# Performance work log

Measured on AMD Instinct MI355X. Metric: run time of the kernel, lower is better.

The kernel has to match this reference:

```python
import math
import jax, jax.numpy as jnp
import numpy as np

HEAD_DIM = 2
ROPE_PERIOD = 19.0
OMEGA = 2.0 * math.pi / ROPE_PERIOD
PEAK_EPS = 0.3
TARGET_LOGIT_GAP = math.log(10.0)
ATTN_AMPLITUDE = TARGET_LOGIT_GAP / (math.cos(OMEGA * PEAK_EPS) - math.cos(OMEGA * (1.0 - PEAK_EPS)))
QK_NORM_SCALE = math.sqrt(ATTN_AMPLITUDE / math.sqrt(2.0))
SCALE = HEAD_DIM ** (-0.5) * QK_NORM_SCALE ** 2
INTERMEDIATE_SIZE = 2
EMBED_CONST = 1000.0
B, L = 4, 4096


def _rms(x, eps=1e-6):
    return x * jax.lax.rsqrt(jnp.mean(x * x, axis=-1, keepdims=True) + eps)


def _rope(x):
    # x: (B, 1, L, 2)
    seq_len = x.shape[2]
    theta = jnp.arange(seq_len, dtype=x.dtype) * jnp.asarray(OMEGA, x.dtype)
    cos_t = jnp.cos(theta)[None, None, :, None]
    sin_t = jnp.sin(theta)[None, None, :, None]
    x0, x1 = x[..., 0:1], x[..., 1:2]
    return jnp.concatenate([x0 * cos_t - x1 * sin_t, x0 * sin_t + x1 * cos_t], axis=-1)


def setup_inputs() -> dict:
    key = jax.random.key(0)
    k1, k2, k3, k4, k5 = jax.random.split(key, 5)
    x = jax.random.normal(k1, (B, L, 2), dtype=jnp.float32)
    # causal additive mask (1, 1, L, L)
    causal = jnp.tril(jnp.ones((L, L), dtype=bool))
    mask = jnp.where(causal, 0.0, -1e9).astype(jnp.float32)[None, None]
    q_weight = jax.random.normal(k2, (1,), dtype=jnp.float32) * 0.1
    v_weight = jax.random.normal(k3, (1,), dtype=jnp.float32) * 0.1
    gate_weight = jax.random.normal(k4, (2,), dtype=jnp.float32) * 0.1
    carry_weight = jax.random.normal(k5, (1,), dtype=jnp.float32) * 0.1
    return {"x": x, "mask": mask, "q_weight": q_weight, "v_weight": v_weight,
            "gate_weight": gate_weight, "carry_weight": carry_weight}


def reference(x, mask, q_weight, v_weight, gate_weight, carry_weight):
    # ---- attention branch ----
    xn = _rms(x)                                    # (B, L, 2)
    phi = q_weight[0]
    q = jnp.stack([xn[..., 0] * jnp.cos(phi), xn[..., 0] * -jnp.sin(phi)], axis=-1)
    k = jnp.stack([xn[..., 0], jnp.zeros_like(xn[..., 0])], axis=-1)
    v = jnp.stack([xn[..., 1] * v_weight[0], jnp.zeros_like(xn[..., 0])], axis=-1)
    q, k, v = q[:, None], k[:, None], v[:, None]    # (B, 1, L, 2)
    q = _rope(_rms(q))
    k = _rope(_rms(k))
    attn = jnp.einsum('bhqd,bhkd->bhqk', q, k) * jnp.asarray(SCALE, x.dtype)
    attn = jax.nn.softmax(attn + mask, axis=-1)
    out = jnp.einsum('bhqk,bhkd->bhqd', attn, v)    # (B, 1, L, 2)
    o0 = out[:, 0, :, 0]                            # (B, L)
    attn_out = jnp.stack([jnp.zeros_like(o0), o0], axis=-1)  # OProj channel swap
    h = x + attn_out
    # ---- gated MLP branch ----
    hn = _rms(h)
    a, c = gate_weight[0], gate_weight[1]
    g0 = hn[..., 0] * a + hn[..., 1] * c
    g1 = hn[..., 0] * (a - c / EMBED_CONST) + hn[..., 1] * c
    base = hn[..., 0]
    mix0 = jax.nn.silu(g0) * base
    mix1 = jax.nn.silu(g1) * base
    y1 = carry_weight[0] * (mix1 - mix0)
    mlp_out = jnp.stack([jnp.zeros_like(y1), y1], axis=-1)
    return h + mlp_out
```

## Files before the change

### kernel.cpp

```cpp
#include <hip/hip_runtime.h>
#include <hip/hip_fp16.h>
#include <math.h>

#define SEQ_L 4096
#define THREADS 512
#define WAVES 8
#define BLOCKS_PER_BATCH 256

__global__ __launch_bounds__(THREADS, 8) void attn_rows_kernel(
    const float* __restrict__ x,
    const float* __restrict__ q_weight,
    const float* __restrict__ v_weight,
    const float* __restrict__ gate_weight,
    const float* __restrict__ carry_weight,
    float* __restrict__ out,
    float scaleL2,
    float cd, float sd,
    float ck1, float sk1,
    float ck2, float sk2,
    float ck3, float sk3)
{
    __shared__ __half2 aw[SEQ_L];

    const int tid  = threadIdx.x;
    const int lane = tid & 63;
    const int wave = tid >> 6;
    const int b    = blockIdx.x >> 8;
    const int bb   = blockIdx.x & 255;

    const float phi = q_weight[0];
    const float vw  = v_weight[0];
    const float2* x2 = (const float2*)x + (size_t)b * SEQ_L;

    const float INV2PI = 0.15915494309189535f;
    const float rphi = phi * INV2PI;
    const float cphi = __builtin_amdgcn_cosf(rphi);
    const float sphi = __builtin_amdgcn_sinf(rphi);

    for (int j = tid; j < SEQ_L; j += THREADS) {
        float2 xv = x2[j];
        float inv = __builtin_amdgcn_rsqf(
                        fmaf(xv.x, xv.x * 0.5f, fmaf(xv.y, xv.y * 0.5f, 1e-6f)));
        float xn0 = xv.x * inv;
        float xn1 = xv.y * inv;
        float a = xn0 * __builtin_amdgcn_rsqf(fmaf(xn0, xn0 * 0.5f, 1e-6f));
        aw[j] = __floats2half2_rn(a, xn1 * vw);
    }
    __syncthreads();

    const float ga = gate_weight[0];
    const float gc = gate_weight[1];
    const float cw = carry_weight[0];

    const int v = bb * WAVES + wave;
    const float SQRT2 = 1.4142135623730951f;
    const float LOG2E = 1.4426950408889634f;
    const float INV19 = 1.0f / 19.0f;

    #pragma unroll
    for (int rr = 0; rr < 2; ++rr) {
        const int i = (rr == 0) ? v : (SEQ_L - 1 - v);

        const float2 xv = x2[i];
        float invx = __builtin_amdgcn_rsqf(
                        fmaf(xv.x, xv.x * 0.5f, fmaf(xv.y, xv.y * 0.5f, 1e-6f)));
        float xn0i = xv.x * invx;
        float a_i  = xn0i * __builtin_amdgcn_rsqf(fmaf(xn0i, xn0i * 0.5f, 1e-6f));
        const float t2 = scaleL2 * a_i;
        const float M2 = fabsf(t2) * SQRT2;

        unsigned r = (unsigned)(i - (lane << 2) + 266) % 19u;
        float rev = (float)r * INV19;
        float cr = __builtin_amdgcn_cosf(rev);
        float sr = __builtin_amdgcn_sinf(rev);
        float c0 = fmaf(sr, sphi, cr * cphi);
        float s0 = fmaf(cr, -sphi, sr * cphi);
        float C = t2 * c0;
        float S = t2 * s0;

        float sA = 0.f, sB = 0.f, oA = 0.f, oB = 0.f;
        int jb = lane << 2;
        const int nfull = (i + 1) >> 8;

        for (int k = 0; k < nfull; ++k) {
            float4 raw = *(const float4*)&aw[jb];
            const __half2* hp = (const __half2*)&raw;
            float2 p0 = __half22float2(hp[0]);
            float2 p1 = __half22float2(hp[1]);
            float2 p2 = __half22float2(hp[2]);
            float2 p3 = __half22float2(hp[3]);
            float C1 = fmaf(S, sk1, C * ck1);
            float C2 = fmaf(S, sk2, C * ck2);
            float C3 = fmaf(S, sk3, C * ck3);
            float e0 = __builtin_amdgcn_exp2f(fmaf(p0.x, C,  -M2));
            float e1 = __builtin_amdgcn_exp2f(fmaf(p1.x, C1, -M2));
            float e2 = __builtin_amdgcn_exp2f(fmaf(p2.x, C2, -M2));
            float e3 = __builtin_amdgcn_exp2f(fmaf(p3.x, C3, -M2));
            sA += e0 + e1;
            sB += e2 + e3;
            oA = fmaf(e0, p0.y, oA);
            oB = fmaf(e1, p1.y, oB);
            oA = fmaf(e2, p2.y, oA);
            oB = fmaf(e3, p3.y, oB);
            float Cn = fmaf(S, sd, C * cd);
            float Sn = fmaf(S, cd, -(C * sd));
            C = Cn; S = Sn;
            jb += 256;
        }
        if ((i & 255) != 255) {
            float4 raw = *(const float4*)&aw[jb];
            const __half2* hp = (const __half2*)&raw;
            float2 p0 = __half22float2(hp[0]);
            float2 p1 = __half22float2(hp[1]);
            float2 p2 = __half22float2(hp[2]);
            float2 p3 = __half22float2(hp[3]);
            float C1 = fmaf(S, sk1, C * ck1);
            float C2 = fmaf(S, sk2, C * ck2);
            float C3 = fmaf(S, sk3, C * ck3);
            float e0 = __builtin_amdgcn_exp2f(fmaf(p0.x, C,  -M2));
            float e1 = __builtin_amdgcn_exp2f(fmaf(p1.x, C1, -M2));
            float e2 = __builtin_amdgcn_exp2f(fmaf(p2.x, C2, -M2));
            float e3 = __builtin_amdgcn_exp2f(fmaf(p3.x, C3, -M2));
            e0 = (jb + 0 <= i) ? e0 : 0.f;
            e1 = (jb + 1 <= i) ? e1 : 0.f;
            e2 = (jb + 2 <= i) ? e2 : 0.f;
            e3 = (jb + 3 <= i) ? e3 : 0.f;
            sA += e0 + e1;
            sB += e2 + e3;
            oA = fmaf(e0, p0.y, oA);
            oB = fmaf(e1, p1.y, oB);
            oA = fmaf(e2, p2.y, oA);
            oB = fmaf(e3, p3.y, oB);
        }

        float ssum = sA + sB;
        float osum = oA + oB;
        for (int off = 32; off > 0; off >>= 1) {
            ssum += __shfl_xor(ssum, off);
            osum += __shfl_xor(osum, off);
        }

        if (lane == 0) {
            float o0 = osum * __builtin_amdgcn_rcpf(ssum);
            float h0 = xv.x;
            float h1 = xv.y + o0;
            float inv = __builtin_amdgcn_rsqf(
                           fmaf(h0, h0 * 0.5f, fmaf(h1, h1 * 0.5f, 1e-6f)));
            float hn0 = h0 * inv, hn1 = h1 * inv;
            float g0 = hn0 * ga + hn1 * gc;
            float g1 = hn0 * (ga - gc * 1e-3f) + hn1 * gc;
            float sig0 = __builtin_amdgcn_rcpf(1.f + __builtin_amdgcn_exp2f(-g0 * LOG2E));
            float sig1 = __builtin_amdgcn_rcpf(1.f + __builtin_amdgcn_exp2f(-g1 * LOG2E));
            float mix0 = g0 * sig0 * hn0;
            float mix1 = g1 * sig1 * hn0;
            float y1 = cw * (mix1 - mix0);
            float2* outp = (float2*)out + (size_t)b * SEQ_L + i;
            *outp = make_float2(xv.x, h1 + y1);
        }
    }
}

extern "C" void kernel_launch(void* const* d_in, const int* in_sizes, int n_in,
                              void* d_out, int out_size, void* d_ws, size_t ws_size,
                              hipStream_t stream)
{
    const float* x  = (const float*)d_in[0];
    const float* qw = (const float*)d_in[2];
    const float* vw = (const float*)d_in[3];
    const float* gw = (const float*)d_in[4];
    const float* cw = (const float*)d_in[5];
    float* out = (float*)d_out;

    const double omega = 2.0 * M_PI / 19.0;
    const double amp   = log(10.0) / (cos(omega * 0.3) - cos(omega * 0.7));
    const double qkns2 = amp / sqrt(2.0);
    const double scale = pow(2.0, -0.5) * qkns2;
    const double L2E   = 1.4426950408889634074;
    const double delta = 256.0 * omega;

    attn_rows_kernel<<<dim3(4 * BLOCKS_PER_BATCH), dim3(THREADS), 0, stream>>>(
        x, qw, vw, gw, cw, out,
        (float)(scale * L2E),
        (float)cos(delta),       (float)sin(delta),
        (float)cos(omega),       (float)sin(omega),
        (float)cos(2.0 * omega), (float)sin(2.0 * omega),
        (float)cos(3.0 * omega), (float)sin(3.0 * omega));
}
```

Before: 19.22 us.

## Process four rows sharing RoPE phase per wave to reuse key loads and rotations

Each wave now handles a group of four query rows whose indices differ by multiples of 19, so they share the same RoPE phase. One set of key loads and cosine rotations then serves all four rows, and the per-row scale folds into a single fma. Groups are paired from both ends of the sequence to balance causal work, the grid is halved with launch bounds relaxed to 4, and the wave reductions use DPP instead of shuffles. In exchange each thread carries more accumulators, which raises register pressure, and the odd group count needs special handling by two waves.

```diff
diff --git a/kernel.cpp b/kernel.cpp
--- a/kernel.cpp
+++ b/kernel.cpp
@@ -4,10 +4,149 @@
 
 #define SEQ_L 4096
 #define THREADS 512
-#define WAVES 8
-#define BLOCKS_PER_BATCH 256
-
-__global__ __launch_bounds__(THREADS, 8) void attn_rows_kernel(
+
+__device__ __forceinline__ float wave_sum_dpp(float x) {
+    int t;
+    t = __builtin_amdgcn_update_dpp(0, __float_as_int(x), 0x111, 0xf, 0xf, true); x += __int_as_float(t);
+    t = __builtin_amdgcn_update_dpp(0, __float_as_int(x), 0x112, 0xf, 0xf, true); x += __int_as_float(t);
+    t = __builtin_amdgcn_update_dpp(0, __float_as_int(x), 0x114, 0xf, 0xf, true); x += __int_as_float(t);
+    t = __builtin_amdgcn_update_dpp(0, __float_as_int(x), 0x118, 0xf, 0xf, true); x += __int_as_float(t);
+    t = __builtin_amdgcn_update_dpp(0, __float_as_int(x), 0x142, 0xa, 0xf, true); x += __int_as_float(t);
+    t = __builtin_amdgcn_update_dpp(0, __float_as_int(x), 0x143, 0xc, 0xf, true); x += __int_as_float(t);
+    return x;
+}
+
+__device__ __forceinline__ void do_group(
+    int g, int lane, const float2* __restrict__ x2, const __half2* aw,
+    float2* __restrict__ outp, float scaleL2, float cphi, float sphi,
+    float cd, float sd, float ck1, float sk1, float ck2, float sk2,
+    float ck3, float sk3, float ga, float gc, float cw)
+{
+    const float INV19 = 1.0f / 19.0f;
+    const float LOG2E = 1.4426950408889634f;
+
+    int m  = g / 19;
+    int c  = g - 19 * m;
+    int b0 = 76 * m + c;
+    int i0r = b0, i1r = b0 + 19, i2r = b0 + 38, i3r = b0 + 57;
+
+    float t2a0, t2a1, t2a2, t2a3, M2a0, M2a1, M2a2, M2a3;
+#define ROWINIT(tk, Mk, ik) { \
+    int ic_ = (ik) < SEQ_L ? (ik) : (SEQ_L - 1); \
+    float2 xv_ = x2[ic_]; \
+    float inv_ = __builtin_amdgcn_rsqf(fmaf(xv_.x, xv_.x*0.5f, fmaf(xv_.y, xv_.y*0.5f, 1e-6f))); \
+    float xn0_ = xv_.x * inv_; \
+    float ai_  = xn0_ * __builtin_amdgcn_rsqf(fmaf(xn0_, xn0_*0.5f, 1e-6f)); \
+    tk = scaleL2 * ai_;  Mk = fabsf(tk) * 1.4142135623730951f; }
+    ROWINIT(t2a0, M2a0, i0r)
+    ROWINIT(t2a1, M2a1, i1r)
+    ROWINIT(t2a2, M2a2, i2r)
+    ROWINIT(t2a3, M2a3, i3r)
+#undef ROWINIT
+
+    unsigned r = (unsigned)(b0 - (lane << 2) + 266) % 19u;
+    float rev = (float)r * INV19;
+    float crv = __builtin_amdgcn_cosf(rev);
+    float srv = __builtin_amdgcn_sinf(rev);
+    float C = fmaf(srv, sphi, crv * cphi);
+    float S = fmaf(crv, -sphi, srv * cphi);
+
+    float sa0=0.f, sa1=0.f, sa2=0.f, sa3=0.f;
+    float oa0=0.f, oa1=0.f, oa2=0.f, oa3=0.f;
+    int jb = lane << 2;
+    const int ncom = (b0 + 1) >> 8;
+    const int i3c  = i3r < SEQ_L ? i3r : (SEQ_L - 1);
+    const int T    = (i3c >> 8) + 1;
+
+#define EL(u, pw) { \
+    float e0_ = __builtin_amdgcn_exp2f(fmaf(t2a0, (u), -M2a0)); \
+    float e1_ = __builtin_amdgcn_exp2f(fmaf(t2a1, (u), -M2a1)); \
+    float e2_ = __builtin_amdgcn_exp2f(fmaf(t2a2, (u), -M2a2)); \
+    float e3_ = __builtin_amdgcn_exp2f(fmaf(t2a3, (u), -M2a3)); \
+    sa0 += e0_; oa0 = fmaf(e0_, (pw), oa0); \
+    sa1 += e1_; oa1 = fmaf(e1_, (pw), oa1); \
+    sa2 += e2_; oa2 = fmaf(e2_, (pw), oa2); \
+    sa3 += e3_; oa3 = fmaf(e3_, (pw), oa3); }
+#define ELM(u, pw, jj) { \
+    float e0_ = __builtin_amdgcn_exp2f(fmaf(t2a0, (u), -M2a0)); \
+    float e1_ = __builtin_amdgcn_exp2f(fmaf(t2a1, (u), -M2a1)); \
+    float e2_ = __builtin_amdgcn_exp2f(fmaf(t2a2, (u), -M2a2)); \
+    float e3_ = __builtin_amdgcn_exp2f(fmaf(t2a3, (u), -M2a3)); \
+    e0_ = ((jj) <= i0r) ? e0_ : 0.f; \
+    e1_ = ((jj) <= i1r) ? e1_ : 0.f; \
+    e2_ = ((jj) <= i2r) ? e2_ : 0.f; \
+    e3_ = ((jj) <= i3r) ? e3_ : 0.f; \
+    sa0 += e0_; oa0 = fmaf(e0_, (pw), oa0); \
+    sa1 += e1_; oa1 = fmaf(e1_, (pw), oa1); \
+    sa2 += e2_; oa2 = fmaf(e2_, (pw), oa2); \
+    sa3 += e3_; oa3 = fmaf(e3_, (pw), oa3); }
+
+    int t = 0;
+    for (; t < ncom; ++t) {
+        float4 raw = *(const float4*)&aw[jb];
+        const __half2* hp = (const __half2*)&raw;
+        float2 p0 = __half22float2(hp[0]);
+        float2 p1 = __half22float2(hp[1]);
+        float2 p2 = __half22float2(hp[2]);
+        float2 p3 = __half22float2(hp[3]);
+        float C1 = fmaf(S, sk1, C * ck1);
+        float C2 = fmaf(S, sk2, C * ck2);
+        float C3 = fmaf(S, sk3, C * ck3);
+        float u0 = p0.x * C,  u1 = p1.x * C1, u2 = p2.x * C2, u3 = p3.x * C3;
+        EL(u0, p0.y) EL(u1, p1.y) EL(u2, p2.y) EL(u3, p3.y)
+        float Cn = fmaf(S, sd, C * cd);
+        float Sn = fmaf(S, cd, -(C * sd));
+        C = Cn; S = Sn;
+        jb += 256;
+    }
+    for (; t < T; ++t) {
+        float4 raw = *(const float4*)&aw[jb];
+        const __half2* hp = (const __half2*)&raw;
+        float2 p0 = __half22float2(hp[0]);
+        float2 p1 = __half22float2(hp[1]);
+        float2 p2 = __half22float2(hp[2]);
+        float2 p3 = __half22float2(hp[3]);
+        float C1 = fmaf(S, sk1, C * ck1);
+        float C2 = fmaf(S, sk2, C * ck2);
+        float C3 = fmaf(S, sk3, C * ck3);
+        float u0 = p0.x * C,  u1 = p1.x * C1, u2 = p2.x * C2, u3 = p3.x * C3;
+        ELM(u0, p0.y, jb)     ELM(u1, p1.y, jb + 1)
+        ELM(u2, p2.y, jb + 2) ELM(u3, p3.y, jb + 3)
+        float Cn = fmaf(S, sd, C * cd);
+        float Sn = fmaf(S, cd, -(C * sd));
+        C = Cn; S = Sn;
+        jb += 256;
+    }
+#undef EL
+#undef ELM
+
+    float S0 = wave_sum_dpp(sa0), O0 = wave_sum_dpp(oa0);
+    float S1 = wave_sum_dpp(sa1), O1 = wave_sum_dpp(oa1);
+    float S2 = wave_sum_dpp(sa2), O2 = wave_sum_dpp(oa2);
+    float S3 = wave_sum_dpp(sa3), O3 = wave_sum_dpp(oa3);
+
+    if (lane == 63) {
+#define EPI(Sk, Ok, ik) if ((ik) < SEQ_L) { \
+    float2 xv_ = x2[ik]; \
+    float o0_ = (Ok) * __builtin_amdgcn_rcpf(Sk); \
+    float h0_ = xv_.x, h1_ = xv_.y + o0_; \
+    float inv_ = __builtin_amdgcn_rsqf(fmaf(h0_, h0_*0.5f, fmaf(h1_, h1_*0.5f, 1e-6f))); \
+    float hn0_ = h0_ * inv_, hn1_ = h1_ * inv_; \
+    float g0_ = hn0_ * ga + hn1_ * gc; \
+    float g1_ = hn0_ * (ga - gc * 1e-3f) + hn1_ * gc; \
+    float sg0_ = __builtin_amdgcn_rcpf(1.f + __builtin_amdgcn_exp2f(-g0_ * LOG2E)); \
+    float sg1_ = __builtin_amdgcn_rcpf(1.f + __builtin_amdgcn_exp2f(-g1_ * LOG2E)); \
+    float y1_ = cw * (g1_ * sg1_ - g0_ * sg0_) * hn0_; \
+    outp[ik] = make_float2(h0_, h1_ + y1_); }
+        EPI(S0, O0, i0r)
+        EPI(S1, O1, i1r)
+        EPI(S2, O2, i2r)
+        EPI(S3, O3, i3r)
+#undef EPI
+    }
+}
+
+__global__ __launch_bounds__(THREADS, 4) void attn_rows_kernel(
     const float* __restrict__ x,
     const float* __restrict__ q_weight,
     const float* __restrict__ v_weight,
@@ -16,21 +155,20 @@
     float* __restrict__ out,
     float scaleL2,
     float cd, float sd,
-    float ck1, float sk1,
-    float ck2, float sk2,
-    float ck3, float sk3)
+    float ck1, float sk1, float ck2, float sk2, float ck3, float sk3)
 {
     __shared__ __half2 aw[SEQ_L];
 
     const int tid  = threadIdx.x;
     const int lane = tid & 63;
     const int wave = tid >> 6;
-    const int b    = blockIdx.x >> 8;
-    const int bb   = blockIdx.x & 255;
+    const int bat  = blockIdx.x >> 7;
+    const int bb   = blockIdx.x & 127;
 
     const float phi = q_weight[0];
     const float vw  = v_weight[0];
-    const float2* x2 = (const float2*)x + (size_t)b * SEQ_L;
+    const float2* x2 = (const float2*)x + (size_t)bat * SEQ_L;
+    float2* outp = (float2*)out + (size_t)bat * SEQ_L;
 
     const float INV2PI = 0.15915494309189535f;
     const float rphi = phi * INV2PI;
@@ -52,112 +190,17 @@
     const float gc = gate_weight[1];
     const float cw = carry_weight[0];
 
-    const int v = bb * WAVES + wave;
-    const float SQRT2 = 1.4142135623730951f;
-    const float LOG2E = 1.4426950408889634f;
-    const float INV19 = 1.0f / 19.0f;
-
-    #pragma unroll
-    for (int rr = 0; rr < 2; ++rr) {
-        const int i = (rr == 0) ? v : (SEQ_L - 1 - v);
-
-        const float2 xv = x2[i];
-        float invx = __builtin_amdgcn_rsqf(
-                        fmaf(xv.x, xv.x * 0.5f, fmaf(xv.y, xv.y * 0.5f, 1e-6f)));
-        float xn0i = xv.x * invx;
-        float a_i  = xn0i * __builtin_amdgcn_rsqf(fmaf(xn0i, xn0i * 0.5f, 1e-6f));
-        const float t2 = scaleL2 * a_i;
-        const float M2 = fabsf(t2) * SQRT2;
-
-        unsigned r = (unsigned)(i - (lane << 2) + 266) % 19u;
-        float rev = (float)r * INV19;
-        float cr = __builtin_amdgcn_cosf(rev);
-        float sr = __builtin_amdgcn_sinf(rev);
-        float c0 = fmaf(sr, sphi, cr * cphi);
-        float s0 = fmaf(cr, -sphi, sr * cphi);
-        float C = t2 * c0;
-        float S = t2 * s0;
-
-        float sA = 0.f, sB = 0.f, oA = 0.f, oB = 0.f;
-        int jb = lane << 2;
-        const int nfull = (i + 1) >> 8;
-
-        for (int k = 0; k < nfull; ++k) {
-            float4 raw = *(const float4*)&aw[jb];
-            const __half2* hp = (const __half2*)&raw;
-            float2 p0 = __half22float2(hp[0]);
-            float2 p1 = __half22float2(hp[1]);
-            float2 p2 = __half22float2(hp[2]);
-            float2 p3 = __half22float2(hp[3]);
-            float C1 = fmaf(S, sk1, C * ck1);
-            float C2 = fmaf(S, sk2, C * ck2);
-            float C3 = fmaf(S, sk3, C * ck3);
-            float e0 = __builtin_amdgcn_exp2f(fmaf(p0.x, C,  -M2));
-            float e1 = __builtin_amdgcn_exp2f(fmaf(p1.x, C1, -M2));
-            float e2 = __builtin_amdgcn_exp2f(fmaf(p2.x, C2, -M2));
-            float e3 = __builtin_amdgcn_exp2f(fmaf(p3.x, C3, -M2));
-            sA += e0 + e1;
-            sB += e2 + e3;
-            oA = fmaf(e0, p0.y, oA);
-            oB = fmaf(e1, p1.y, oB);
-            oA = fmaf(e2, p2.y, oA);
-            oB = fmaf(e3, p3.y, oB);
-            float Cn = fmaf(S, sd, C * cd);
-            float Sn = fmaf(S, cd, -(C * sd));
-            C = Cn; S = Sn;
-            jb += 256;
-        }
-        if ((i & 255) != 255) {
-            float4 raw = *(const float4*)&aw[jb];
-            const __half2* hp = (const __half2*)&raw;
-            float2 p0 = __half22float2(hp[0]);
-            float2 p1 = __half22float2(hp[1]);
-            float2 p2 = __half22float2(hp[2]);
-            float2 p3 = __half22float2(hp[3]);
-            float C1 = fmaf(S, sk1, C * ck1);
-            float C2 = fmaf(S, sk2, C * ck2);
-            float C3 = fmaf(S, sk3, C * ck3);
-            float e0 = __builtin_amdgcn_exp2f(fmaf(p0.x, C,  -M2));
-            float e1 = __builtin_amdgcn_exp2f(fmaf(p1.x, C1, -M2));
-            float e2 = __builtin_amdgcn_exp2f(fmaf(p2.x, C2, -M2));
-            float e3 = __builtin_amdgcn_exp2f(fmaf(p3.x, C3, -M2));
-            e0 = (jb + 0 <= i) ? e0 : 0.f;
-            e1 = (jb + 1 <= i) ? e1 : 0.f;
-            e2 = (jb + 2 <= i) ? e2 : 0.f;
-            e3 = (jb + 3 <= i) ? e3 : 0.f;
-            sA += e0 + e1;
-            sB += e2 + e3;
-            oA = fmaf(e0, p0.y, oA);
-            oB = fmaf(e1, p1.y, oB);
-            oA = fmaf(e2, p2.y, oA);
-            oB = fmaf(e3, p3.y, oB);
-        }
-
-        float ssum = sA + sB;
-        float osum = oA + oB;
-        for (int off = 32; off > 0; off >>= 1) {
-            ssum += __shfl_xor(ssum, off);
-            osum += __shfl_xor(osum, off);
-        }
-
-        if (lane == 0) {
-            float o0 = osum * __builtin_amdgcn_rcpf(ssum);
-            float h0 = xv.x;
-            float h1 = xv.y + o0;
-            float inv = __builtin_amdgcn_rsqf(
-                           fmaf(h0, h0 * 0.5f, fmaf(h1, h1 * 0.5f, 1e-6f)));
-            float hn0 = h0 * inv, hn1 = h1 * inv;
-            float g0 = hn0 * ga + hn1 * gc;
-            float g1 = hn0 * (ga - gc * 1e-3f) + hn1 * gc;
-            float sig0 = __builtin_amdgcn_rcpf(1.f + __builtin_amdgcn_exp2f(-g0 * LOG2E));
-            float sig1 = __builtin_amdgcn_rcpf(1.f + __builtin_amdgcn_exp2f(-g1 * LOG2E));
-            float mix0 = g0 * sig0 * hn0;
-            float mix1 = g1 * sig1 * hn0;
-            float y1 = cw * (mix1 - mix0);
-            float2* outp = (float2*)out + (size_t)b * SEQ_L + i;
-            *outp = make_float2(xv.x, h1 + y1);
-        }
-    }
+    const int q = bb + (wave << 7);
+    const int g = (q < 513) ? q : (1538 - q);
+
+    do_group(g, lane, x2, aw, outp, scaleL2, cphi, sphi,
+             cd, sd, ck1, sk1, ck2, sk2, ck3, sk3, ga, gc, cw);
+    if (q == 511)
+        do_group(514, lane, x2, aw, outp, scaleL2, cphi, sphi,
+                 cd, sd, ck1, sk1, ck2, sk2, ck3, sk3, ga, gc, cw);
+    else if (q == 512)
+        do_group(513, lane, x2, aw, outp, scaleL2, cphi, sphi,
+                 cd, sd, ck1, sk1, ck2, sk2, ck3, sk3, ga, gc, cw);
 }
 
 extern "C" void kernel_launch(void* const* d_in, const int* in_sizes, int n_in,
@@ -178,7 +221,7 @@
     const double L2E   = 1.4426950408889634074;
     const double delta = 256.0 * omega;
 
-    attn_rows_kernel<<<dim3(4 * BLOCKS_PER_BATCH), dim3(THREADS), 0, stream>>>(
+    attn_rows_kernel<<<dim3(4 * 128), dim3(THREADS), 0, stream>>>(
         x, qw, vw, gw, cw, out,
         (float)(scale * L2E),
         (float)cos(delta),       (float)sin(delta),
```

Measured after the change: 18.41 us. 4.2% less time.
